# Kernel tuning notes

Measured on AMD Instinct MI355X. Metric: run time of the kernel, lower is better.

## Reference

```python
import jax, jax.numpy as jnp
import numpy as np

_pi = np.pi
CONST_FACTOR = np.array([
    1/np.sqrt(4*_pi),
    2*_pi/3*np.sqrt(3/(4*_pi)), 2*_pi/3*np.sqrt(3/(4*_pi)), 2*_pi/3*np.sqrt(3/(4*_pi)),
    _pi/4*3*np.sqrt(5/(12*_pi)), _pi/4*3*np.sqrt(5/(12*_pi)), _pi/4*3*np.sqrt(5/(12*_pi)),
    _pi/4*(3/2)*np.sqrt(5/(12*_pi)), _pi/4*(1/2)*np.sqrt(5/(4*_pi))], dtype=np.float32)


def setup_inputs() -> dict:
    key = jax.random.key(0)
    ks = jax.random.split(key, 8)
    B, V, F, H, W, U = 4, 5023, 9976, 512, 512, 256
    vertices = jax.random.normal(ks[0], (B, V, 3), jnp.float32)
    transformed_vertices = jax.random.normal(ks[1], (B, V, 3), jnp.float32)
    albedos = jax.random.uniform(ks[2], (B, 3, U, U), jnp.float32)
    lights = jax.random.normal(ks[3], (B, 9, 3), jnp.float32) * 0.3
    faces = jax.random.randint(ks[4], (F, 3), 0, V, jnp.int32)
    face_uvcoords = jax.random.uniform(ks[5], (1, F, 3, 3), jnp.float32, minval=-1.0, maxval=1.0)
    # rasterizer outputs (external CUDA kernel): -1 == no face hit
    pix_to_face = jax.random.randint(ks[6], (B, H, W, 1), 0, F + 1, jnp.int32) - 1
    b = jax.random.uniform(ks[7], (B, H, W, 1, 3), jnp.float32) + 1e-3
    bary_coords = b / b.sum(-1, keepdims=True)
    return dict(vertices=vertices, transformed_vertices=transformed_vertices,
                albedos=albedos, lights=lights, face_uvcoords=face_uvcoords,
                bary_coords=bary_coords, faces=faces, pix_to_face=pix_to_face)


def _vertex_normals(vertices, faces):
    vf = vertices[:, faces]                    # [B,F,3,3] face-vertex gather
    v0, v1, v2 = vf[:, :, 0], vf[:, :, 1], vf[:, :, 2]
    B, V = vertices.shape[:2]
    n = jnp.zeros((B, V, 3), vertices.dtype)
    n = n.at[:, faces[:, 1]].add(jnp.cross(v2 - v1, v0 - v1))
    n = n.at[:, faces[:, 2]].add(jnp.cross(v0 - v2, v1 - v2))
    n = n.at[:, faces[:, 0]].add(jnp.cross(v1 - v0, v2 - v0))
    return n / jnp.clip(jnp.linalg.norm(n, axis=-1, keepdims=True), 1e-6)


def _grid_sample(img, grid):
    # torch F.grid_sample bilinear, align_corners=False, zero padding
    # img [B,C,Hi,Wi], grid [B,Ho,Wo,2] (x,y) in [-1,1]
    B, C, Hi, Wi = img.shape
    x = (grid[..., 0] + 1.0) * (Wi * 0.5) - 0.5
    y = (grid[..., 1] + 1.0) * (Hi * 0.5) - 0.5
    x0 = jnp.floor(x); y0 = jnp.floor(y)
    wx = x - x0; wy = y - y0

    def fetch(xi, yi):
        xi_i = xi.astype(jnp.int32); yi_i = yi.astype(jnp.int32)
        valid = ((xi_i >= 0) & (xi_i < Wi) & (yi_i >= 0) & (yi_i < Hi)).astype(img.dtype)
        xc = jnp.clip(xi_i, 0, Wi - 1); yc = jnp.clip(yi_i, 0, Hi - 1)
        vals = jax.vmap(lambda im, yy, xx: im[:, yy, xx])(img, yc, xc)  # [B,C,Ho,Wo]
        return vals * valid[:, None]

    return (fetch(x0, y0) * ((1 - wx) * (1 - wy))[:, None]
            + fetch(x0 + 1, y0) * (wx * (1 - wy))[:, None]
            + fetch(x0, y0 + 1) * ((1 - wx) * wy)[:, None]
            + fetch(x0 + 1, y0 + 1) * (wx * wy)[:, None])


def reference(vertices, transformed_vertices, albedos, lights, face_uvcoords,
              bary_coords, faces, pix_to_face):
    sg = jax.lax.stop_gradient
    B = vertices.shape[0]
    cf = jnp.asarray(CONST_FACTOR)

    # depth normalization (global min/max as in torch)
    z = transformed_vertices[:, :, 2]
    z = z - z.min(); z = z / z.max(); z = z * 80.0 + 10.0
    tv = transformed_vertices.at[:, :, 2].set(z)

    face_vertice = vertices[:, faces]                        # [B,F,3,3]
    normals = _vertex_normals(vertices, faces)
    face_normals = normals[:, faces]                         # [B,F,3,3]
    t_normals = _vertex_normals(tv, faces)
    t_face_normals = t_normals[:, faces]                     # [B,F,3,3]

    attributes = jnp.concatenate([
        jnp.broadcast_to(face_uvcoords, (B,) + face_uvcoords.shape[1:]),
        sg(t_face_normals), sg(face_vertice), face_normals], -1)  # [B,F,3,12]

    # barycentric interpolation (Pytorch3dRasterizer.forward tail)
    mask = pix_to_face < 0                                   # [B,H,W,1]
    safe = jnp.where(mask, 0, pix_to_face)
    pfv = attributes[jnp.arange(B)[:, None, None, None], safe]   # [B,H,W,1,3,12]
    pv = (bary_coords[..., None] * pfv).sum(-2)              # [B,H,W,1,12]
    pv = jnp.where(mask[..., None], 0.0, pv)
    pv = pv[:, :, :, 0].transpose(0, 3, 1, 2)                # [B,12,H,W]
    vismask = (~mask[..., 0]).astype(pv.dtype)[:, None]      # [B,1,H,W]
    rendering = jnp.concatenate([pv, vismask], 1)            # [B,13,H,W]

    # albedo sampling via UV grid
    grid = rendering[:, :2].transpose(0, 2, 3, 1)            # [B,H,W,2]
    albedo_images = _grid_sample(albedos, grid)              # [B,3,H,W]

    # spherical harmonic shading (add_SHlight, lights [B,9,3])
    N = rendering[:, 9:12]                                   # [B,3,H,W]
    one = jnp.ones_like(N[:, 0])
    sh = jnp.stack([one, N[:, 0], N[:, 1], N[:, 2],
                    N[:, 0] * N[:, 1], N[:, 0] * N[:, 2], N[:, 1] * N[:, 2],
                    N[:, 0] ** 2 - N[:, 1] ** 2, 3.0 * N[:, 2] ** 2 - 1.0], 1)  # [B,9,H,W]
    sh = sh * cf[None, :, None, None]
    shading = (lights[:, :, :, None, None] * sh[:, :, None]).sum(1)  # [B,3,H,W]

    images = albedo_images * shading
    return images
```

## Files before the change

### kernel.cpp

```cpp
#include <hip/hip_runtime.h>
#include <hip/hip_fp16.h>
#include <math.h>

#define NB 4
#define NV 5023
#define NF 9976
#define NH 512
#define NW 512
#define NU 256

__device__ __constant__ float d_cf[9] = {
    0.28209479177387814f,
    1.0233267079464885f,
    1.0233267079464885f,
    1.0233267079464885f,
    0.8580855308091875f,
    0.8580855308091875f,
    0.8580855308091875f,
    0.42904276540459376f,
    0.24770795610037571f
};

#define NRM_FLOATS  (NB * NV * 3)
#define ZERO_BLOCKS ((NRM_FLOATS + 255) / 256)
#define FACE_ITEMS  (NB * NF)
#define FACE_BLOCKS ((FACE_ITEMS + 255) / 256)

#define ACELLS 257
#define AINT2_ITEMS  (NB * ACELLS * ACELLS)
#define AINT2_BLOCKS ((AINT2_ITEMS + 255) / 256)

__device__ inline float pack2h(float a, float b) {
    __half2 h = __halves2half2(__float2half_rn(a), __float2half_rn(b));
    union { __half2 h; float f; } u; u.h = h; return u.f;
}
__device__ inline float2 unpack2h(float f) {
    union { float f; __half2 h; } u; u.f = f;
    return __half22float2(u.h);
}
__device__ inline float pack2s(float a, float b) {
    unsigned int lo = (unsigned short)(short)__float2int_rn(a * 32767.0f);
    unsigned int hi = (unsigned short)(short)__float2int_rn(b * 32767.0f);
    return __uint_as_float(lo | (hi << 16));
}
__device__ inline float2 unpack2s(float f) {
    unsigned int u = __float_as_uint(f);
    const float s = 1.0f / 32767.0f;
    return make_float2((float)(short)(u & 0xffffu) * s,
                       (float)(short)(u >> 16) * s);
}
__device__ inline unsigned int packu10(float r, float g, float b) {
    unsigned int qr = (unsigned int)__float2int_rn(r * 1023.0f);
    unsigned int qg = (unsigned int)__float2int_rn(g * 1023.0f);
    unsigned int qb = (unsigned int)__float2int_rn(b * 1023.0f);
    return qr | (qg << 10) | (qb << 20);
}

__global__ void init_kernel(float*       __restrict__ nrm,
                            const float* __restrict__ albedos,
                            const float* __restrict__ lights,
                            uint4*       __restrict__ aint2,
                            float*       __restrict__ lsbuf) {
    if (blockIdx.x < ZERO_BLOCKS) {
        int i = blockIdx.x * blockDim.x + threadIdx.x;
        if (i < NRM_FLOATS) nrm[i] = 0.0f;
        if (i < NB * 27) {
            int b = i / 27;
            int kc = i - b * 27;
            lsbuf[i] = lights[b * 27 + kc] * d_cf[kc / 3];
        }
    } else {
        int j = (blockIdx.x - ZERO_BLOCKS) * blockDim.x + threadIdx.x;
        if (j >= AINT2_ITEMS) return;
        int b = j / (ACELLS * ACELLS);
        int rc = j - b * (ACELLS * ACELLS);
        int r = rc / ACELLS;
        int c = rc - r * ACELLS;

        const float* ab = albedos + (size_t)b * 3 * NU * NU;
        uint4 cell = make_uint4(0u, 0u, 0u, 0u);

        int x0 = c - 1, x1 = c;
        int y0 = r - 1, y1 = r;
        bool vx0 = (x0 >= 0);
        bool vx1 = (x1 <= NU - 1);
        bool vy0 = (y0 >= 0);
        bool vy1 = (y1 <= NU - 1);

        if (vy0) {
            int row = y0 * NU;
            if (vx0) { int o = row + x0;
                cell.x = packu10(ab[o], ab[NU*NU + o], ab[2*NU*NU + o]); }
            if (vx1) { int o = row + x1;
                cell.y = packu10(ab[o], ab[NU*NU + o], ab[2*NU*NU + o]); }
        }
        if (vy1) {
            int row = y1 * NU;
            if (vx0) { int o = row + x0;
                cell.z = packu10(ab[o], ab[NU*NU + o], ab[2*NU*NU + o]); }
            if (vx1) { int o = row + x1;
                cell.w = packu10(ab[o], ab[NU*NU + o], ab[2*NU*NU + o]); }
        }
        aint2[j] = cell;
    }
}

__global__ void face_accum_kernel(const float* __restrict__ verts,
                                  const int*   __restrict__ faces,
                                  float*       __restrict__ nrm) {
    int idx = blockIdx.x * blockDim.x + threadIdx.x;
    if (idx >= FACE_ITEMS) return;
    int b = idx / NF;
    int f = idx - b * NF;

    int i0 = faces[f * 3 + 0];
    int i1 = faces[f * 3 + 1];
    int i2 = faces[f * 3 + 2];

    const float* vb = verts + (size_t)b * NV * 3;
    float v0x = vb[i0 * 3 + 0], v0y = vb[i0 * 3 + 1], v0z = vb[i0 * 3 + 2];
    float v1x = vb[i1 * 3 + 0], v1y = vb[i1 * 3 + 1], v1z = vb[i1 * 3 + 2];
    float v2x = vb[i2 * 3 + 0], v2y = vb[i2 * 3 + 1], v2z = vb[i2 * 3 + 2];

    float ax = v1x - v0x, ay = v1y - v0y, az = v1z - v0z;
    float bx = v2x - v0x, by = v2y - v0y, bz = v2z - v0z;
    float cx = ay * bz - az * by;
    float cy = az * bx - ax * bz;
    float cz = ax * by - ay * bx;

    float* nb = nrm + (size_t)b * NV * 3;
    atomicAdd(&nb[i0 * 3 + 0], cx);
    atomicAdd(&nb[i0 * 3 + 1], cy);
    atomicAdd(&nb[i0 * 3 + 2], cz);
    atomicAdd(&nb[i1 * 3 + 0], cx);
    atomicAdd(&nb[i1 * 3 + 1], cy);
    atomicAdd(&nb[i1 * 3 + 2], cz);
    atomicAdd(&nb[i2 * 3 + 0], cx);
    atomicAdd(&nb[i2 * 3 + 1], cy);
    atomicAdd(&nb[i2 * 3 + 2], cz);
}

__global__ void pack_kernel(const float* __restrict__ nrm,
                            const int*   __restrict__ faces,
                            const float* __restrict__ uvc,
                            float4*      __restrict__ recs) {
    int idx = blockIdx.x * blockDim.x + threadIdx.x;
    if (idx >= FACE_ITEMS) return;
    int b = idx / NF;
    int f = idx - b * NF;

    int i0 = faces[f * 3 + 0];
    int i1 = faces[f * 3 + 1];
    int i2 = faces[f * 3 + 2];

    const float* nb = nrm + (size_t)b * NV * 3;
    float n0x = nb[i0 * 3 + 0], n0y = nb[i0 * 3 + 1], n0z = nb[i0 * 3 + 2];
    float n1x = nb[i1 * 3 + 0], n1y = nb[i1 * 3 + 1], n1z = nb[i1 * 3 + 2];
    float n2x = nb[i2 * 3 + 0], n2y = nb[i2 * 3 + 1], n2z = nb[i2 * 3 + 2];

    float l0 = 1.0f / fmaxf(sqrtf(n0x*n0x + n0y*n0y + n0z*n0z), 1e-6f);
    float l1 = 1.0f / fmaxf(sqrtf(n1x*n1x + n1y*n1y + n1z*n1z), 1e-6f);
    float l2 = 1.0f / fmaxf(sqrtf(n2x*n2x + n2y*n2y + n2z*n2z), 1e-6f);

    const float* uvf = uvc + (size_t)f * 9;

    float4 q0, q1;
    q0.x = pack2s(uvf[0], uvf[1]);
    q0.y = pack2s(uvf[3], uvf[4]);
    q0.z = pack2s(uvf[6], uvf[7]);
    q0.w = pack2h(n0x * l0, n0y * l0);
    q1.x = pack2h(n0z * l0, n1x * l1);
    q1.y = pack2h(n1y * l1, n1z * l1);
    q1.z = pack2h(n2x * l2, n2y * l2);
    q1.w = pack2h(n2z * l2, 0.0f);

    recs[(size_t)idx * 2 + 0] = q0;
    recs[(size_t)idx * 2 + 1] = q1;
}

__global__ void render_kernel(const float4* __restrict__ recs,
                              const uint4* __restrict__ aint2,
                              const float* __restrict__ lsbuf,
                              const float4* __restrict__ bary4,
                              const int4*  __restrict__ p2f4,
                              float*       __restrict__ out) {
    const int blk = blockIdx.x;
    const int xcd = blk & 7;
    const int b   = xcd >> 1;
    const int j   = ((blk >> 3) << 1) | (xcd & 1);
    const int q   = j * 256 + threadIdx.x;
    const int p   = q * 4;

    const int pixq = (b * NH * NW) / 4 + q;
    const int4 f4 = p2f4[pixq];
    const float4 bq0 = bary4[pixq * 3 + 0];
    const float4 bq1 = bary4[pixq * 3 + 1];
    const float4 bq2 = bary4[pixq * 3 + 2];

    const float* Ls = lsbuf + b * 27;

    const int fs[4] = {f4.x, f4.y, f4.z, f4.w};
    const float bw[12] = {bq0.x, bq0.y, bq0.z,  bq0.w, bq1.x, bq1.y,
                          bq1.z, bq1.w, bq2.x,  bq2.y, bq2.z, bq2.w};

    const float4* rb = recs + (size_t)b * NF * 2;
    const uint4* ab = aint2 + (size_t)b * ACELLS * ACELLS;

    float outv[3][4];
    const float inv1023 = 1.0f / 1023.0f;

    #pragma unroll
    for (int px = 0; px < 4; ++px) {
        const int f = fs[px];
        float b0 = bw[px * 3 + 0], b1 = bw[px * 3 + 1], b2 = bw[px * 3 + 2];

        float u = 0.f, v = 0.f, nx = 0.f, ny = 0.f, nz = 0.f;
        if (f >= 0) {
            float4 q0 = rb[(size_t)f * 2 + 0];
            float4 q1 = rb[(size_t)f * 2 + 1];
            float2 uv0 = unpack2s(q0.x);
            float2 uv1 = unpack2s(q0.y);
            float2 uv2 = unpack2s(q0.z);
            float2 hA  = unpack2h(q0.w);
            float2 hB  = unpack2h(q1.x);
            float2 hC  = unpack2h(q1.y);
            float2 hD  = unpack2h(q1.z);
            float2 hE  = unpack2h(q1.w);

            u  = b0 * uv0.x + b1 * uv1.x + b2 * uv2.x;
            v  = b0 * uv0.y + b1 * uv1.y + b2 * uv2.y;
            nx = b0 * hA.x + b1 * hB.y + b2 * hD.x;
            ny = b0 * hA.y + b1 * hC.x + b2 * hD.y;
            nz = b0 * hB.x + b1 * hC.y + b2 * hE.x;
        }

        float x = (u + 1.0f) * (NU * 0.5f) - 0.5f;
        float y = (v + 1.0f) * (NU * 0.5f) - 0.5f;
        float x0f = floorf(x);
        float y0f = floorf(y);
        float wx = x - x0f;
        float wy = y - y0f;
        int ci = (int)x0f + 1;
        int ri = (int)y0f + 1;

        uint4 cell = ab[ri * ACELLS + ci];

        float iwx = 1.0f - wx, iwy = 1.0f - wy;
        float w00 = iwx * iwy, w10 = wx * iwy, w01 = iwx * wy, w11 = wx * wy;

        float a0 = w00 * (float)(cell.x & 1023u)
                 + w10 * (float)(cell.y & 1023u)
                 + w01 * (float)(cell.z & 1023u)
                 + w11 * (float)(cell.w & 1023u);
        float a1 = w00 * (float)((cell.x >> 10) & 1023u)
                 + w10 * (float)((cell.y >> 10) & 1023u)
                 + w01 * (float)((cell.z >> 10) & 1023u)
                 + w11 * (float)((cell.w >> 10) & 1023u);
        float a2 = w00 * (float)((cell.x >> 20) & 1023u)
                 + w10 * (float)((cell.y >> 20) & 1023u)
                 + w01 * (float)((cell.z >> 20) & 1023u)
                 + w11 * (float)((cell.w >> 20) & 1023u);
        a0 *= inv1023; a1 *= inv1023; a2 *= inv1023;

        float sh[9];
        sh[0] = 1.0f;
        sh[1] = nx;
        sh[2] = ny;
        sh[3] = nz;
        sh[4] = nx * ny;
        sh[5] = nx * nz;
        sh[6] = ny * nz;
        sh[7] = nx * nx - ny * ny;
        sh[8] = 3.0f * nz * nz - 1.0f;

        float s0 = 0.f, s1 = 0.f, s2 = 0.f;
        #pragma unroll
        for (int k = 0; k < 9; ++k) {
            s0 += Ls[k * 3 + 0] * sh[k];
            s1 += Ls[k * 3 + 1] * sh[k];
            s2 += Ls[k * 3 + 2] * sh[k];
        }

        outv[0][px] = a0 * s0;
        outv[1][px] = a1 * s1;
        outv[2][px] = a2 * s2;
    }

    const size_t hw = (size_t)NH * NW;
    #pragma unroll
    for (int c = 0; c < 3; ++c) {
        float4* op = (float4*)(out + ((size_t)b * 3 + c) * hw + p);
        *op = make_float4(outv[c][0], outv[c][1], outv[c][2], outv[c][3]);
    }
}

extern "C" void kernel_launch(void* const* d_in, const int* in_sizes, int n_in,
                              void* d_out, int out_size, void* d_ws, size_t ws_size,
                              hipStream_t stream) {
    const float* vertices = (const float*)d_in[0];
    const float* albedos  = (const float*)d_in[2];
    const float* lights   = (const float*)d_in[3];
    const float* uvc      = (const float*)d_in[4];
    const float* bary     = (const float*)d_in[5];
    const int*   faces    = (const int*)d_in[6];
    const int*   p2f      = (const int*)d_in[7];
    float*       out      = (float*)d_out;

    char* ws = (char*)d_ws;
    float* nrm = (float*)ws;
    size_t nrm_bytes = (size_t)NB * NV * 3 * sizeof(float);
    size_t off = (nrm_bytes + 255) & ~(size_t)255;
    float4* recs = (float4*)(ws + off);
    off += (size_t)FACE_ITEMS * 32;
    off = (off + 255) & ~(size_t)255;
    uint4* aint2 = (uint4*)(ws + off);
    off += (size_t)AINT2_ITEMS * sizeof(uint4);
    off = (off + 255) & ~(size_t)255;
    float* lsbuf = (float*)(ws + off);

    {
        init_kernel<<<ZERO_BLOCKS + AINT2_BLOCKS, 256, 0, stream>>>(
            nrm, albedos, lights, aint2, lsbuf);
    }
    {
        face_accum_kernel<<<FACE_BLOCKS, 256, 0, stream>>>(vertices, faces, nrm);
    }
    {
        pack_kernel<<<FACE_BLOCKS, 256, 0, stream>>>(nrm, faces, uvc, recs);
    }
    {
        render_kernel<<<NB * 256, 256, 0, stream>>>(recs, aint2, lsbuf,
                                                    (const float4*)bary,
                                                    (const int4*)p2f, out);
    }
}
```

Baseline: 48.95 us.

## Shrink init to a vectorized zero pass and fuse albedo prep into pack kernel

```diff
diff --git a/kernel.cpp b/kernel.cpp
--- a/kernel.cpp
+++ b/kernel.cpp
@@ -22,13 +22,14 @@
 };
 
 #define NRM_FLOATS  (NB * NV * 3)
-#define ZERO_BLOCKS ((NRM_FLOATS + 255) / 256)
 #define FACE_ITEMS  (NB * NF)
-#define FACE_BLOCKS ((FACE_ITEMS + 255) / 256)
 
 #define ACELLS 257
 #define AINT2_ITEMS  (NB * ACELLS * ACELLS)
-#define AINT2_BLOCKS ((AINT2_ITEMS + 255) / 256)
+
+#define LS_ITEMS     (NB * 27)
+#define PACK_BLOCKS  ((FACE_ITEMS + LS_ITEMS + 63) / 64)
+#define ALB_BLOCKS   ((AINT2_ITEMS + 63) / 64)
 
 __device__ inline float pack2h(float a, float b) {
     __half2 h = __halves2half2(__float2half_rn(a), __float2half_rn(b));
@@ -56,53 +57,9 @@
     return qr | (qg << 10) | (qb << 20);
 }
 
-__global__ void init_kernel(float*       __restrict__ nrm,
-                            const float* __restrict__ albedos,
-                            const float* __restrict__ lights,
-                            uint4*       __restrict__ aint2,
-                            float*       __restrict__ lsbuf) {
-    if (blockIdx.x < ZERO_BLOCKS) {
-        int i = blockIdx.x * blockDim.x + threadIdx.x;
-        if (i < NRM_FLOATS) nrm[i] = 0.0f;
-        if (i < NB * 27) {
-            int b = i / 27;
-            int kc = i - b * 27;
-            lsbuf[i] = lights[b * 27 + kc] * d_cf[kc / 3];
-        }
-    } else {
-        int j = (blockIdx.x - ZERO_BLOCKS) * blockDim.x + threadIdx.x;
-        if (j >= AINT2_ITEMS) return;
-        int b = j / (ACELLS * ACELLS);
-        int rc = j - b * (ACELLS * ACELLS);
-        int r = rc / ACELLS;
-        int c = rc - r * ACELLS;
-
-        const float* ab = albedos + (size_t)b * 3 * NU * NU;
-        uint4 cell = make_uint4(0u, 0u, 0u, 0u);
-
-        int x0 = c - 1, x1 = c;
-        int y0 = r - 1, y1 = r;
-        bool vx0 = (x0 >= 0);
-        bool vx1 = (x1 <= NU - 1);
-        bool vy0 = (y0 >= 0);
-        bool vy1 = (y1 <= NU - 1);
-
-        if (vy0) {
-            int row = y0 * NU;
-            if (vx0) { int o = row + x0;
-                cell.x = packu10(ab[o], ab[NU*NU + o], ab[2*NU*NU + o]); }
-            if (vx1) { int o = row + x1;
-                cell.y = packu10(ab[o], ab[NU*NU + o], ab[2*NU*NU + o]); }
-        }
-        if (vy1) {
-            int row = y1 * NU;
-            if (vx0) { int o = row + x0;
-                cell.z = packu10(ab[o], ab[NU*NU + o], ab[2*NU*NU + o]); }
-            if (vx1) { int o = row + x1;
-                cell.w = packu10(ab[o], ab[NU*NU + o], ab[2*NU*NU + o]); }
-        }
-        aint2[j] = cell;
-    }
+__global__ void zero_kernel(float4* __restrict__ nrm4) {
+    int i = blockIdx.x * blockDim.x + threadIdx.x;
+    if (i < NRM_FLOATS / 4) nrm4[i] = make_float4(0.f, 0.f, 0.f, 0.f);
 }
 
 __global__ void face_accum_kernel(const float* __restrict__ verts,
@@ -140,42 +97,86 @@
     atomicAdd(&nb[i2 * 3 + 2], cz);
 }
 
-__global__ void pack_kernel(const float* __restrict__ nrm,
-                            const int*   __restrict__ faces,
-                            const float* __restrict__ uvc,
-                            float4*      __restrict__ recs) {
-    int idx = blockIdx.x * blockDim.x + threadIdx.x;
-    if (idx >= FACE_ITEMS) return;
-    int b = idx / NF;
-    int f = idx - b * NF;
-
-    int i0 = faces[f * 3 + 0];
-    int i1 = faces[f * 3 + 1];
-    int i2 = faces[f * 3 + 2];
-
-    const float* nb = nrm + (size_t)b * NV * 3;
-    float n0x = nb[i0 * 3 + 0], n0y = nb[i0 * 3 + 1], n0z = nb[i0 * 3 + 2];
-    float n1x = nb[i1 * 3 + 0], n1y = nb[i1 * 3 + 1], n1z = nb[i1 * 3 + 2];
-    float n2x = nb[i2 * 3 + 0], n2y = nb[i2 * 3 + 1], n2z = nb[i2 * 3 + 2];
-
-    float l0 = 1.0f / fmaxf(sqrtf(n0x*n0x + n0y*n0y + n0z*n0z), 1e-6f);
-    float l1 = 1.0f / fmaxf(sqrtf(n1x*n1x + n1y*n1y + n1z*n1z), 1e-6f);
-    float l2 = 1.0f / fmaxf(sqrtf(n2x*n2x + n2y*n2y + n2z*n2z), 1e-6f);
-
-    const float* uvf = uvc + (size_t)f * 9;
-
-    float4 q0, q1;
-    q0.x = pack2s(uvf[0], uvf[1]);
-    q0.y = pack2s(uvf[3], uvf[4]);
-    q0.z = pack2s(uvf[6], uvf[7]);
-    q0.w = pack2h(n0x * l0, n0y * l0);
-    q1.x = pack2h(n0z * l0, n1x * l1);
-    q1.y = pack2h(n1y * l1, n1z * l1);
-    q1.z = pack2h(n2x * l2, n2y * l2);
-    q1.w = pack2h(n2z * l2, 0.0f);
-
-    recs[(size_t)idx * 2 + 0] = q0;
-    recs[(size_t)idx * 2 + 1] = q1;
+__global__ void pack_alb_kernel(const float* __restrict__ nrm,
+                                const int*   __restrict__ faces,
+                                const float* __restrict__ uvc,
+                                const float* __restrict__ albedos,
+                                const float* __restrict__ lights,
+                                float4*      __restrict__ recs,
+                                uint4*       __restrict__ aint2,
+                                float*       __restrict__ lsbuf) {
+    if (blockIdx.x < PACK_BLOCKS) {
+        int idx = blockIdx.x * blockDim.x + threadIdx.x;
+        if (idx < FACE_ITEMS) {
+            int b = idx / NF;
+            int f = idx - b * NF;
+
+            int i0 = faces[f * 3 + 0];
+            int i1 = faces[f * 3 + 1];
+            int i2 = faces[f * 3 + 2];
+
+            const float* nb = nrm + (size_t)b * NV * 3;
+            float n0x = nb[i0*3+0], n0y = nb[i0*3+1], n0z = nb[i0*3+2];
+            float n1x = nb[i1*3+0], n1y = nb[i1*3+1], n1z = nb[i1*3+2];
+            float n2x = nb[i2*3+0], n2y = nb[i2*3+1], n2z = nb[i2*3+2];
+
+            float l0 = 1.0f / fmaxf(sqrtf(n0x*n0x + n0y*n0y + n0z*n0z), 1e-6f);
+            float l1 = 1.0f / fmaxf(sqrtf(n1x*n1x + n1y*n1y + n1z*n1z), 1e-6f);
+            float l2 = 1.0f / fmaxf(sqrtf(n2x*n2x + n2y*n2y + n2z*n2z), 1e-6f);
+
+            const float* uvf = uvc + (size_t)f * 9;
+
+            float4 q0, q1;
+            q0.x = pack2s(uvf[0], uvf[1]);
+            q0.y = pack2s(uvf[3], uvf[4]);
+            q0.z = pack2s(uvf[6], uvf[7]);
+            q0.w = pack2h(n0x * l0, n0y * l0);
+            q1.x = pack2h(n0z * l0, n1x * l1);
+            q1.y = pack2h(n1y * l1, n1z * l1);
+            q1.z = pack2h(n2x * l2, n2y * l2);
+            q1.w = pack2h(n2z * l2, 0.0f);
+
+            recs[(size_t)idx * 2 + 0] = q0;
+            recs[(size_t)idx * 2 + 1] = q1;
+        } else if (idx < FACE_ITEMS + LS_ITEMS) {
+            int i = idx - FACE_ITEMS;
+            int kc = i % 27;
+            lsbuf[i] = lights[i] * d_cf[kc / 3];
+        }
+    } else {
+        int j = (blockIdx.x - PACK_BLOCKS) * blockDim.x + threadIdx.x;
+        if (j >= AINT2_ITEMS) return;
+        int b = j / (ACELLS * ACELLS);
+        int rc = j - b * (ACELLS * ACELLS);
+        int r = rc / ACELLS;
+        int c = rc - r * ACELLS;
+
+        const float* ab = albedos + (size_t)b * 3 * NU * NU;
+        uint4 cell = make_uint4(0u, 0u, 0u, 0u);
+
+        int x0 = c - 1, x1 = c;
+        int y0 = r - 1, y1 = r;
+        bool vx0 = (x0 >= 0);
+        bool vx1 = (x1 <= NU - 1);
+        bool vy0 = (y0 >= 0);
+        bool vy1 = (y1 <= NU - 1);
+
+        if (vy0) {
+            int row = y0 * NU;
+            if (vx0) { int o = row + x0;
+                cell.x = packu10(ab[o], ab[NU*NU + o], ab[2*NU*NU + o]); }
+            if (vx1) { int o = row + x1;
+                cell.y = packu10(ab[o], ab[NU*NU + o], ab[2*NU*NU + o]); }
+        }
+        if (vy1) {
+            int row = y1 * NU;
+            if (vx0) { int o = row + x0;
+                cell.z = packu10(ab[o], ab[NU*NU + o], ab[2*NU*NU + o]); }
+            if (vx1) { int o = row + x1;
+                cell.w = packu10(ab[o], ab[NU*NU + o], ab[2*NU*NU + o]); }
+        }
+        aint2[j] = cell;
+    }
 }
 
 __global__ void render_kernel(const float4* __restrict__ recs,
@@ -319,14 +320,15 @@
     float* lsbuf = (float*)(ws + off);
 
     {
-        init_kernel<<<ZERO_BLOCKS + AINT2_BLOCKS, 256, 0, stream>>>(
-            nrm, albedos, lights, aint2, lsbuf);
+        zero_kernel<<<(NRM_FLOATS / 4 + 255) / 256, 256, 0, stream>>>((float4*)nrm);
     }
     {
-        face_accum_kernel<<<FACE_BLOCKS, 256, 0, stream>>>(vertices, faces, nrm);
+        face_accum_kernel<<<(FACE_ITEMS + 63) / 64, 64, 0, stream>>>(
+            vertices, faces, nrm);
     }
     {
-        pack_kernel<<<FACE_BLOCKS, 256, 0, stream>>>(nrm, faces, uvc, recs);
+        pack_alb_kernel<<<PACK_BLOCKS + ALB_BLOCKS, 64, 0, stream>>>(
+            nrm, faces, uvc, albedos, lights, recs, aint2, lsbuf);
     }
     {
         render_kernel<<<NB * 256, 256, 0, stream>>>(recs, aint2, lsbuf,
```

Result: slower. 51.92 us (+6.1%).
